# Optimization experiments

Hardware: AMD Instinct MI355X
Metric: run time of the kernel (lower is better)

## Reference

```python
import jax, jax.numpy as jnp
import numpy as np

MU_P = 0.15
MASK_ID = 103
VOCAB = 30522


def setup_inputs() -> dict:
    key = jax.random.key(0)
    k1, k2 = jax.random.split(key)
    B, C, S = 1024, 4, 2048
    # first half = per-token sampling weights, second half = shared_tokens (unused by the math)
    my_attention_mask = jax.random.uniform(k1, (B, C, 2 * S), dtype=jnp.float32)
    attention_mask = jnp.ones((B, C, S), dtype=jnp.int32)  # tokenizer attention mask
    input_ids = jax.random.randint(k2, (B, C, S), 0, VOCAB, dtype=jnp.int32)
    return {"my_attention_mask": my_attention_mask,
            "attention_mask": attention_mask,
            "input_ids": input_ids}


def reference(my_attention_mask, attention_mask, input_ids):
    """Weighted sampling WITHOUT replacement per (batch, choice) row via Gumbel-top-k.

    Original loops over (k, j), draws num_to_mask = floor(sum(tok_mask) * N(mu_p, sigma))
    indices from the nonzero weights in my_attention_mask[..., :S] (prob ~ weight),
    masks those token positions in input_ids and emits the indicator mask.
    Gumbel-top-k: keys = log(w) + Gumbel noise; the top-num_to_mask keys are a
    weighted sample without replacement from w. Zero-weight positions get -inf keys.
    """
    B, C, S = input_ids.shape
    w = my_attention_mask[..., :S]  # [B, C, S] sampling weights

    key = jax.random.key(42)
    kg, kn = jax.random.split(key)
    sigma = min(0.05, MU_P / 4.0)
    frac = MU_P + sigma * jax.random.normal(kn, (B, C), dtype=jnp.float32)
    num_to_mask = jnp.floor(
        attention_mask.sum(axis=-1).astype(jnp.float32) * frac
    ).astype(jnp.int32)  # [B, C]

    log_w = jnp.where(w > 0, jnp.log(jnp.maximum(w, 1e-30)), -jnp.inf)
    keys = log_w + jax.random.gumbel(kg, w.shape, dtype=jnp.float32)  # [B, C, S]

    # rank[i] = position of i in descending key order (double argsort)
    order = jnp.argsort(-keys, axis=-1)
    rank = jnp.argsort(order, axis=-1)
    new_attention_mask = (rank < num_to_mask[..., None]).astype(jnp.int32)  # [B, C, S]

    new_input_ids = jnp.where(new_attention_mask == 1, MASK_ID, input_ids)
    discriminator_labels = -new_attention_mask
    return new_input_ids, new_attention_mask, discriminator_labels
```

## Files before the change

kernel.cpp:

```cpp
#include <hip/hip_runtime.h>
#include <stdint.h>
#include <math.h>

#define SLEN 2048
#define EPT 16
#define NTHREADS 128
#define CPW 4
#define TOKENS_PER_OUT 8388608

__host__ __device__ __forceinline__ void tf2x32(uint32_t k0, uint32_t k1,
                                                uint32_t x0, uint32_t x1,
                                                uint32_t &o0, uint32_t &o1) {
  uint32_t ks2 = 0x1BD11BDAu ^ k0 ^ k1;
  x0 += k0; x1 += k1;
#define TFR(r) { x0 += x1; x1 = (x1 << (r)) | (x1 >> (32 - (r))); x1 ^= x0; }
  TFR(13) TFR(15) TFR(26) TFR(6)
  x0 += k1;  x1 += ks2 + 1u;
  TFR(17) TFR(29) TFR(16) TFR(24)
  x0 += ks2; x1 += k0 + 2u;
  TFR(13) TFR(15) TFR(26) TFR(6)
  x0 += k0;  x1 += k1 + 3u;
  TFR(17) TFR(29) TFR(16) TFR(24)
  x0 += k1;  x1 += ks2 + 4u;
  TFR(13) TFR(15) TFR(26) TFR(6)
  x0 += ks2; x1 += k0 + 5u;
#undef TFR
  o0 = x0; o1 = x1;
}

__device__ __forceinline__ void tf4_bits(uint32_t k0, uint32_t k1,
                                         uint32_t cbase, uint32_t bits[4]) {
  const uint32_t ks2 = 0x1BD11BDAu ^ k0 ^ k1;
  uint32_t x0[4], x1[4];
#pragma unroll
  for (int i = 0; i < 4; ++i) { x0[i] = k0; x1[i] = (cbase + (uint32_t)i) + k1; }
#define TFR4(r)                                                         \
  _Pragma("unroll")                                                     \
  for (int i = 0; i < 4; ++i) {                                         \
    x0[i] += x1[i];                                                     \
    x1[i] = (x1[i] << (r)) | (x1[i] >> (32 - (r)));                     \
    x1[i] ^= x0[i];                                                     \
  }                                                                     \
  __builtin_amdgcn_sched_barrier(0);
#define INJ4(a, b)                                                      \
  _Pragma("unroll")                                                     \
  for (int i = 0; i < 4; ++i) { x0[i] += (a); x1[i] += (b); }
  TFR4(13) TFR4(15) TFR4(26) TFR4(6)
  INJ4(k1, ks2 + 1u)
  TFR4(17) TFR4(29) TFR4(16) TFR4(24)
  INJ4(ks2, k0 + 2u)
  TFR4(13) TFR4(15) TFR4(26) TFR4(6)
  INJ4(k0, k1 + 3u)
  TFR4(17) TFR4(29) TFR4(16) TFR4(24)
  INJ4(k1, ks2 + 4u)
  TFR4(13) TFR4(15) TFR4(26) TFR4(6)
  INJ4(ks2, k0 + 5u)
#undef TFR4
#undef INJ4
#pragma unroll
  for (int i = 0; i < 4; ++i) bits[i] = x0[i] ^ x1[i];
}

__device__ __forceinline__ float u01_from_bits(uint32_t bits) {
  return __uint_as_float((bits >> 9) | 0x3F800000u) - 1.0f;
}

#define SBAR() __builtin_amdgcn_sched_barrier(0)

__device__ __forceinline__ void log8_cr(const float x[8], float out[8]) {
#pragma clang fp contract(off)
  double m[8]; int e[8];
#pragma unroll
  for (int i = 0; i < 8; ++i) {
    uint32_t xb   = __float_as_uint(x[i]);
    uint32_t mant = xb & 0x7FFFFFu;
    int      ee   = (int)(xb >> 23) - 127;
    bool     big  = mant > 0x3504F3u;
    e[i] = ee + (big ? 1 : 0);
    uint32_t hi = (big ? 0x3FE00000u : 0x3FF00000u) | (mant >> 3);
    uint32_t lo = mant << 29;
    m[i] = __longlong_as_double(((long long)hi << 32) | (long long)lo);
  }
  SBAR();
  double mp1[8];
#pragma unroll
  for (int i = 0; i < 8; ++i) mp1[i] = m[i] + 1.0;
  SBAR();
  double y[8];
#pragma unroll
  for (int i = 0; i < 8; ++i) y[i] = __builtin_amdgcn_rcp(mp1[i]);
  SBAR();
#pragma unroll
  for (int i = 0; i < 8; ++i) y[i] = fma(fma(-mp1[i], y[i], 1.0), y[i], y[i]);
  SBAR();
  double r[8];
#pragma unroll
  for (int i = 0; i < 8; ++i) r[i] = (m[i] - 1.0) * y[i];
  SBAR();
  double t[8];
#pragma unroll
  for (int i = 0; i < 8; ++i) t[i] = r[i] * r[i];
  SBAR();
  double p[8];
#pragma unroll
  for (int i = 0; i < 8; ++i) p[i] = fma(0.07692307692307693, t[i], 0.09090909090909091);
  SBAR();
#pragma unroll
  for (int i = 0; i < 8; ++i) p[i] = fma(p[i], t[i], 0.1111111111111111);
  SBAR();
#pragma unroll
  for (int i = 0; i < 8; ++i) p[i] = fma(p[i], t[i], 0.14285714285714285);
  SBAR();
#pragma unroll
  for (int i = 0; i < 8; ++i) p[i] = fma(p[i], t[i], 0.2);
  SBAR();
#pragma unroll
  for (int i = 0; i < 8; ++i) p[i] = fma(p[i], t[i], 0.3333333333333333);
  SBAR();
#pragma unroll
  for (int i = 0; i < 8; ++i) p[i] = fma(p[i], t[i], 1.0);
  SBAR();
#pragma unroll
  for (int i = 0; i < 8; ++i) r[i] = r[i] + r[i];
  SBAR();
#pragma unroll
  for (int i = 0; i < 8; ++i) p[i] = r[i] * p[i];
  SBAR();
#pragma unroll
  for (int i = 0; i < 8; ++i)
    out[i] = (float)fma((double)e[i], 0.6931471805599453, p[i]);
}

__device__ __forceinline__ float log_cr(float x) {
#pragma clang fp contract(off)
  uint32_t xb   = __float_as_uint(x);
  uint32_t mant = xb & 0x7FFFFFu;
  int      e    = (int)(xb >> 23) - 127;
  bool     big  = mant > 0x3504F3u;
  e += big ? 1 : 0;
  uint32_t hi = (big ? 0x3FE00000u : 0x3FF00000u) | (mant >> 3);
  double m = __longlong_as_double(((long long)hi << 32) | (long long)(mant << 29));
  double mp1 = m + 1.0;
  double y = __builtin_amdgcn_rcp(mp1);
  y = fma(fma(-mp1, y, 1.0), y, y);
  double r = (m - 1.0) * y;
  double t = r * r;
  double p = fma(0.07692307692307693, t, 0.09090909090909091);
  p = fma(p, t, 0.1111111111111111);
  p = fma(p, t, 0.14285714285714285);
  p = fma(p, t, 0.2);
  p = fma(p, t, 0.3333333333333333);
  p = fma(p, t, 1.0);
  return (float)fma((double)e, 0.6931471805599453, (r + r) * p);
}

__device__ float erfinv_xla(float x) {
#pragma clang fp contract(off)
  float x2  = x * x;
  float nx2 = -x2;
  float l1p;
  if (fabsf(nx2) < 1e-4f) {
    l1p = (-0.5f * nx2 + 1.0f) * nx2;
  } else {
    l1p = log_cr(1.0f + nx2);
  }
  float w = -l1p;
  float p;
  if (w < 5.0f) {
    float ww = w - 2.5f;
    p = 2.81022636e-08f;
    p = p * ww + 3.43273939e-07f;
    p = p * ww + -3.5233877e-06f;
    p = p * ww + -4.39150654e-06f;
    p = p * ww + 0.00021858087f;
    p = p * ww + -0.00125372503f;
    p = p * ww + -0.00417768164f;
    p = p * ww + 0.246640727f;
    p = p * ww + 1.50140941f;
  } else {
    float ww = sqrtf(w) - 3.0f;
    p = -0.000200214257f;
    p = p * ww + 0.000100950558f;
    p = p * ww + 0.00134934322f;
    p = p * ww + -0.00367342844f;
    p = p * ww + 0.00573950773f;
    p = p * ww + -0.0076224613f;
    p = p * ww + 0.00943887047f;
    p = p * ww + 1.00167406f;
    p = p * ww + 2.83297682f;
  }
  return p * x;
}

__global__ __launch_bounds__(NTHREADS, 8)
void gumbel_topk_mask(const float* __restrict__ wfull,
                      const int*   __restrict__ attn,
                      const int*   __restrict__ ids,
                      int* __restrict__ out,
                      uint32_t kg0, uint32_t kg1, uint32_t kn0, uint32_t kn1) {
#pragma clang fp contract(off)
  const int t    = threadIdx.x;
  const int lane = t & 63;
  const int wid  = t >> 6;
  const int row  = blockIdx.x;

  __shared__ __align__(16) uint32_t hist[2][256];
  __shared__ uint32_t wsum[2];
  __shared__ uint32_t wtot[2];

  const size_t rbase = (size_t)row * SLEN;
  const size_t wbase = (size_t)row * (2 * SLEN);

  ((uint2*)hist[0])[64 * wid + lane] = make_uint2(0u, 0u);

  const int4*   av4 = (const int4*)(attn + rbase);
  const float4* wv4 = (const float4*)(wfull + wbase);
  const int4*   iv4 = (const int4*)(ids + rbase);

  int psum = 0;
#pragma unroll
  for (int j = 0; j < CPW; ++j) {
    int4 a = av4[64 * (CPW * wid + j) + lane];
    psum += a.x + a.y + a.z + a.w;
  }

  uint32_t no0, no1;
  tf2x32(kn0, kn1, 0u, (uint32_t)row, no0, no1);
  float f0  = u01_from_bits(no0 ^ no1);
  float lo  = __uint_as_float(0xBF7FFFFFu);
  float u2  = fmaxf(lo, f0 * 2.0f + lo);
  float z   = erfinv_xla(u2);
  float nrm = 1.4142135623730951f * z;
  float frac = 0.15f + 0.0375f * nrm;

#pragma unroll
  for (int off = 32; off; off >>= 1) psum += __shfl_down(psum, off, 64);
  if (lane == 0) wsum[wid] = (uint32_t)psum;

  uint32_t mloc[EPT];
#pragma unroll
  for (int c = 0; c < 2; ++c) {
    const int g0 = CPW * wid + 2 * c;
    float4 wa = wv4[64 * g0 + lane];
    float4 wb = wv4[64 * (g0 + 1) + lane];
    uint32_t bits[8];
    tf4_bits(kg0, kg1, (uint32_t)(rbase + 256 * g0 + 4 * lane), bits + 0);
    tf4_bits(kg0, kg1, (uint32_t)(rbase + 256 * (g0 + 1) + 4 * lane), bits + 4);
    SBAR();
    float wl[8] = {wa.x, wa.y, wa.z, wa.w, wb.x, wb.y, wb.z, wb.w};
    float uu[8];
#pragma unroll
    for (int e = 0; e < 8; ++e) {
      float f = u01_from_bits(bits[e]);
      uu[e] = fmaxf(1.17549435e-38f, f * 1.0f + 1.17549435e-38f);
    }
    SBAR();
    float l1[8];
    log8_cr(uu, l1);
    float wm[8];
#pragma unroll
    for (int e = 0; e < 8; ++e) wm[e] = fmaxf(wl[e], 1e-30f);
    float lw[8];
    log8_cr(wm, lw);
    float nl1[8];
#pragma unroll
    for (int e = 0; e < 8; ++e) nl1[e] = -l1[e];
    float l2[8];
    log8_cr(nl1, l2);
    SBAR();
#pragma unroll
    for (int e = 0; e < 8; ++e) {
      float key = (wl[e] > 0.0f) ? (lw[e] + (-l2[e])) : -__builtin_inff();
      uint32_t kb = __float_as_uint(key);
      mloc[8 * c + e] = (kb & 0x80000000u) ? ~kb : (kb | 0x80000000u);
    }
  }

  int4 idsv[CPW];
#pragma unroll
  for (int j = 0; j < CPW; ++j) idsv[j] = iv4[64 * (CPW * wid + j) + lane];

  __syncthreads();
  int asum = (int)(wsum[0] + wsum[1]);
  int kk = (int)floorf((float)asum * frac);

  uint32_t T, r;
  if (kk <= 0)          { T = 0xFFFFFFFFu; r = 0u; }
  else if (kk >= SLEN)  { T = 0u;          r = (uint32_t)SLEN; }
  else {
    T = 0u;
    uint32_t need = (uint32_t)kk;
#pragma unroll
    for (int e = 0; e < EPT; ++e)
      atomicAdd(&hist[0][mloc[e] >> 24], 1u);
    int cur = 0;
    for (int p = 3; ; --p) {
      __syncthreads();
      uint4 hq = ((const uint4*)hist[cur])[lane];
      ((uint2*)hist[cur ^ 1])[64 * wid + lane] = make_uint2(0u, 0u);
      uint32_t gs  = hq.x + hq.y + hq.z + hq.w;
      uint32_t sfx = gs;
#pragma unroll
      for (int off = 1; off < 64; off <<= 1) {
        uint32_t n = __shfl_down(sfx, off, 64);
        if (lane + off < 64) sfx += n;
      }
      uint32_t Gex = sfx - gs;
      uint32_t S3 = Gex;
      uint32_t S2 = S3 + hq.w;
      uint32_t S1 = S2 + hq.z;
      uint32_t S0 = S1 + hq.y;
      uint32_t hh[4] = {hq.x, hq.y, hq.z, hq.w};
      uint32_t SS[4] = {S0, S1, S2, S3};
      int haswin = 0; uint32_t binv = 0u, remv = 0u; int donev = 0;
#pragma unroll
      for (int i = 0; i < 4; ++i) {
        if (hh[i] && SS[i] < need && need <= SS[i] + hh[i]) {
          haswin = 1;
          binv = (uint32_t)(4 * lane + i);
          remv = need - SS[i];
          donev = (remv == hh[i]) ? 1 : 0;
        }
      }
      unsigned long long wmask = __ballot(haswin);
      int src = (int)(__ffsll((unsigned long long)wmask) - 1);
      uint32_t bin = (uint32_t)__shfl((int)binv, src, 64);
      uint32_t rem = (uint32_t)__shfl((int)remv, src, 64);
      int     done = __shfl(donev, src, 64);
      T |= bin << (8 * p);
      need = rem;
      if (done || p == 0) { r = rem; break; }
      __syncthreads();
      const int sh = 8 * p;
#pragma unroll
      for (int e = 0; e < EPT; ++e) {
        uint32_t m = mloc[e];
        if ((m >> sh) == (T >> sh))
          atomicAdd(&hist[cur ^ 1][(m >> (sh - 8)) & 255u], 1u);
      }
      cur ^= 1;
    }
  }

  uint32_t cnt[CPW];
#pragma unroll
  for (int j = 0; j < CPW; ++j) {
    uint32_t c = 0;
#pragma unroll
    for (int e = 0; e < 4; ++e) c += (mloc[4 * j + e] == T) ? 1u : 0u;
    cnt[j] = c;
  }
  uint32_t incl[2];
#pragma unroll
  for (int q = 0; q < 2; ++q) incl[q] = cnt[2 * q] | (cnt[2 * q + 1] << 16);
#pragma unroll
  for (int off = 1; off < 64; off <<= 1) {
#pragma unroll
    for (int q = 0; q < 2; ++q) {
      uint32_t n = __shfl_up(incl[q], off, 64);
      if (lane >= off) incl[q] += n;
    }
  }
  uint32_t Spre[CPW], tot[CPW];
#pragma unroll
  for (int q = 0; q < 2; ++q) {
    uint32_t t63 = (uint32_t)__shfl((int)incl[q], 63, 64);
    tot[2 * q]      = t63 & 0xFFFFu;
    tot[2 * q + 1]  = t63 >> 16;
    Spre[2 * q]     = (incl[q] & 0xFFFFu) - cnt[2 * q];
    Spre[2 * q + 1] = (incl[q] >> 16)     - cnt[2 * q + 1];
  }
  if (lane == 0) wtot[wid] = tot[0] + tot[1] + tot[2] + tot[3];
  __syncthreads();
  uint32_t C = wid ? wtot[0] : 0u;

  int4* po = (int4*)(out + rbase);
  int4* pm = (int4*)(out + TOKENS_PER_OUT + rbase);
  int4* pl = (int4*)(out + 2 * TOKENS_PER_OUT + rbase);
#pragma unroll
  for (int j = 0; j < CPW; ++j) {
    uint32_t excl = C + Spre[j];
    int4 iv = idsv[j];
    int idv[4] = {iv.x, iv.y, iv.z, iv.w};
    int oid[4], omk[4], olb[4];
#pragma unroll
    for (int e = 0; e < 4; ++e) {
      uint32_t m = mloc[4 * j + e];
      bool eq  = (m == T);
      bool msk = (m > T) || (eq && (excl < r));
      excl += eq ? 1u : 0u;
      oid[e] = msk ? 103 : idv[e];
      omk[e] = msk ? 1 : 0;
      olb[e] = msk ? -1 : 0;
    }
    const int gi = 64 * (CPW * wid + j) + lane;
    po[gi] = make_int4(oid[0], oid[1], oid[2], oid[3]);
    pm[gi] = make_int4(omk[0], omk[1], omk[2], omk[3]);
    pl[gi] = make_int4(olb[0], olb[1], olb[2], olb[3]);
    C += tot[j];
  }
}

extern "C" void kernel_launch(void* const* d_in, const int* in_sizes, int n_in,
                              void* d_out, int out_size, void* d_ws, size_t ws_size,
                              hipStream_t stream) {
  (void)n_in; (void)d_ws; (void)ws_size; (void)out_size;
  const float* wfull = (const float*)d_in[0];
  const int*   attn  = (const int*)d_in[1];
  const int*   ids   = (const int*)d_in[2];
  int* out = (int*)d_out;

  uint32_t kg0, kg1, kn0, kn1, o0, o1;
  tf2x32(0u, 42u, 0u, 0u, o0, o1); kg0 = o0; kg1 = o1;
  tf2x32(0u, 42u, 0u, 1u, o0, o1); kn0 = o0; kn1 = o1;

  int rows = in_sizes[1] / SLEN;
  hipLaunchKernelGGL(gumbel_topk_mask, dim3(rows), dim3(NTHREADS),
                     0, stream, wfull, attn, ids, out, kg0, kg1, kn0, kn1);
}
```

Before: 213.1 us.

## Process four rows per wave pair with register prefetch of next row

Each block now runs two independent wave pairs, each handling four consecutive rows. The inputs for the next row are prefetched into registers while the current row is being computed. The intent is to hide global load latency and to amortise launch and block setup. The cost is more register pressure, with launch bounds dropped to 2 blocks, and fewer blocks overall (1024 rows / 8 = 512), which risks lower occupancy and block-wide barriers shared across both pairs.

```diff
diff --git a/kernel.cpp b/kernel.cpp
--- a/kernel.cpp
+++ b/kernel.cpp
@@ -4,8 +4,9 @@
 
 #define SLEN 2048
 #define EPT 16
-#define NTHREADS 128
+#define NTHREADS 256
 #define CPW 4
+#define DSEQ 4
 #define TOKENS_PER_OUT 8388608
 
 __host__ __device__ __forceinline__ void tf2x32(uint32_t k0, uint32_t k1,
@@ -192,7 +193,7 @@
   return p * x;
 }
 
-__global__ __launch_bounds__(NTHREADS, 8)
+__global__ __launch_bounds__(NTHREADS, 2)
 void gumbel_topk_mask(const float* __restrict__ wfull,
                       const int*   __restrict__ attn,
                       const int*   __restrict__ ids,
@@ -202,202 +203,237 @@
   const int t    = threadIdx.x;
   const int lane = t & 63;
   const int wid  = t >> 6;
-  const int row  = blockIdx.x;
-
-  __shared__ __align__(16) uint32_t hist[2][256];
-  __shared__ uint32_t wsum[2];
-  __shared__ uint32_t wtot[2];
-
-  const size_t rbase = (size_t)row * SLEN;
-  const size_t wbase = (size_t)row * (2 * SLEN);
-
-  ((uint2*)hist[0])[64 * wid + lane] = make_uint2(0u, 0u);
-
-  const int4*   av4 = (const int4*)(attn + rbase);
-  const float4* wv4 = (const float4*)(wfull + wbase);
-  const int4*   iv4 = (const int4*)(ids + rbase);
-
-  int psum = 0;
-#pragma unroll
-  for (int j = 0; j < CPW; ++j) {
-    int4 a = av4[64 * (CPW * wid + j) + lane];
-    psum += a.x + a.y + a.z + a.w;
+  const int pid  = wid >> 1;
+  const int wl   = wid & 1;
+
+  __shared__ __align__(16) uint32_t hist[2][2][256];
+  __shared__ uint32_t wsum[2][2];
+  __shared__ uint32_t wtot[2][2];
+
+  const int row0 = (blockIdx.x * 2 + pid) * DSEQ;
+
+  int4 attnC[CPW]; float4 wC[CPW]; int4 idsC[CPW];
+  {
+    const size_t rb = (size_t)row0 * SLEN;
+    const int4*   av4 = (const int4*)(attn + rb);
+    const float4* wv4 = (const float4*)(wfull + 2 * rb);
+    const int4*   iv4 = (const int4*)(ids + rb);
+#pragma unroll
+    for (int j = 0; j < CPW; ++j) {
+      attnC[j] = av4[64 * (CPW * wl + j) + lane];
+      wC[j]    = wv4[64 * (CPW * wl + j) + lane];
+      idsC[j]  = iv4[64 * (CPW * wl + j) + lane];
+    }
   }
 
-  uint32_t no0, no1;
-  tf2x32(kn0, kn1, 0u, (uint32_t)row, no0, no1);
-  float f0  = u01_from_bits(no0 ^ no1);
-  float lo  = __uint_as_float(0xBF7FFFFFu);
-  float u2  = fmaxf(lo, f0 * 2.0f + lo);
-  float z   = erfinv_xla(u2);
-  float nrm = 1.4142135623730951f * z;
-  float frac = 0.15f + 0.0375f * nrm;
-
-#pragma unroll
-  for (int off = 32; off; off >>= 1) psum += __shfl_down(psum, off, 64);
-  if (lane == 0) wsum[wid] = (uint32_t)psum;
-
-  uint32_t mloc[EPT];
-#pragma unroll
-  for (int c = 0; c < 2; ++c) {
-    const int g0 = CPW * wid + 2 * c;
-    float4 wa = wv4[64 * g0 + lane];
-    float4 wb = wv4[64 * (g0 + 1) + lane];
-    uint32_t bits[8];
-    tf4_bits(kg0, kg1, (uint32_t)(rbase + 256 * g0 + 4 * lane), bits + 0);
-    tf4_bits(kg0, kg1, (uint32_t)(rbase + 256 * (g0 + 1) + 4 * lane), bits + 4);
-    SBAR();
-    float wl[8] = {wa.x, wa.y, wa.z, wa.w, wb.x, wb.y, wb.z, wb.w};
-    float uu[8];
-#pragma unroll
-    for (int e = 0; e < 8; ++e) {
-      float f = u01_from_bits(bits[e]);
-      uu[e] = fmaxf(1.17549435e-38f, f * 1.0f + 1.17549435e-38f);
-    }
-    SBAR();
-    float l1[8];
-    log8_cr(uu, l1);
-    float wm[8];
-#pragma unroll
-    for (int e = 0; e < 8; ++e) wm[e] = fmaxf(wl[e], 1e-30f);
-    float lw[8];
-    log8_cr(wm, lw);
-    float nl1[8];
-#pragma unroll
-    for (int e = 0; e < 8; ++e) nl1[e] = -l1[e];
-    float l2[8];
-    log8_cr(nl1, l2);
-    SBAR();
-#pragma unroll
-    for (int e = 0; e < 8; ++e) {
-      float key = (wl[e] > 0.0f) ? (lw[e] + (-l2[e])) : -__builtin_inff();
-      uint32_t kb = __float_as_uint(key);
-      mloc[8 * c + e] = (kb & 0x80000000u) ? ~kb : (kb | 0x80000000u);
-    }
-  }
-
-  int4 idsv[CPW];
-#pragma unroll
-  for (int j = 0; j < CPW; ++j) idsv[j] = iv4[64 * (CPW * wid + j) + lane];
-
-  __syncthreads();
-  int asum = (int)(wsum[0] + wsum[1]);
-  int kk = (int)floorf((float)asum * frac);
-
-  uint32_t T, r;
-  if (kk <= 0)          { T = 0xFFFFFFFFu; r = 0u; }
-  else if (kk >= SLEN)  { T = 0u;          r = (uint32_t)SLEN; }
-  else {
-    T = 0u;
-    uint32_t need = (uint32_t)kk;
-#pragma unroll
-    for (int e = 0; e < EPT; ++e)
-      atomicAdd(&hist[0][mloc[e] >> 24], 1u);
+  for (int rr = 0; rr < DSEQ; ++rr) {
+    const int row = row0 + rr;
+    const size_t rbase = (size_t)row * SLEN;
+
+    int4 attnN[CPW]; float4 wN[CPW]; int4 idsN[CPW];
+    if (rr < DSEQ - 1) {
+      const size_t rbN = rbase + SLEN;
+      const int4*   av4 = (const int4*)(attn + rbN);
+      const float4* wv4 = (const float4*)(wfull + 2 * rbN);
+      const int4*   iv4 = (const int4*)(ids + rbN);
+#pragma unroll
+      for (int j = 0; j < CPW; ++j) {
+        attnN[j] = av4[64 * (CPW * wl + j) + lane];
+        wN[j]    = wv4[64 * (CPW * wl + j) + lane];
+        idsN[j]  = iv4[64 * (CPW * wl + j) + lane];
+      }
+    }
+
+    ((uint2*)hist[pid][0])[64 * wl + lane] = make_uint2(0u, 0u);
+
+    int psum = 0;
+#pragma unroll
+    for (int j = 0; j < CPW; ++j)
+      psum += attnC[j].x + attnC[j].y + attnC[j].z + attnC[j].w;
+
+    uint32_t no0, no1;
+    tf2x32(kn0, kn1, 0u, (uint32_t)row, no0, no1);
+    float f0  = u01_from_bits(no0 ^ no1);
+    float lo  = __uint_as_float(0xBF7FFFFFu);
+    float u2  = fmaxf(lo, f0 * 2.0f + lo);
+    float z   = erfinv_xla(u2);
+    float nrm = 1.4142135623730951f * z;
+    float frac = 0.15f + 0.0375f * nrm;
+
+#pragma unroll
+    for (int off = 32; off; off >>= 1) psum += __shfl_down(psum, off, 64);
+    if (lane == 0) wsum[pid][wl] = (uint32_t)psum;
+
+    uint32_t mloc[EPT];
+#pragma unroll
+    for (int c = 0; c < 2; ++c) {
+      const int g0 = CPW * wl + 2 * c;
+      float4 wa = wC[2 * c], wb = wC[2 * c + 1];
+      uint32_t bits[8];
+      tf4_bits(kg0, kg1, (uint32_t)(rbase + 256 * g0 + 4 * lane), bits + 0);
+      tf4_bits(kg0, kg1, (uint32_t)(rbase + 256 * (g0 + 1) + 4 * lane), bits + 4);
+      SBAR();
+      float wl8[8] = {wa.x, wa.y, wa.z, wa.w, wb.x, wb.y, wb.z, wb.w};
+      float uu[8];
+#pragma unroll
+      for (int e = 0; e < 8; ++e) {
+        float f = u01_from_bits(bits[e]);
+        uu[e] = fmaxf(1.17549435e-38f, f * 1.0f + 1.17549435e-38f);
+      }
+      SBAR();
+      float l1[8];
+      log8_cr(uu, l1);
+      float wm[8];
+#pragma unroll
+      for (int e = 0; e < 8; ++e) wm[e] = fmaxf(wl8[e], 1e-30f);
+      float lw[8];
+      log8_cr(wm, lw);
+      float nl1[8];
+#pragma unroll
+      for (int e = 0; e < 8; ++e) nl1[e] = -l1[e];
+      float l2[8];
+      log8_cr(nl1, l2);
+      SBAR();
+#pragma unroll
+      for (int e = 0; e < 8; ++e) {
+        float key = (wl8[e] > 0.0f) ? (lw[e] + (-l2[e])) : -__builtin_inff();
+        uint32_t kb = __float_as_uint(key);
+        mloc[8 * c + e] = (kb & 0x80000000u) ? ~kb : (kb | 0x80000000u);
+      }
+    }
+
+    __syncthreads();
+    int asum = (int)(wsum[pid][0] + wsum[pid][1]);
+    int kk = (int)floorf((float)asum * frac);
+
+    uint32_t T = 0u, r = 0u, need = 0u;
+    bool doneF = false;
+    if (kk <= 0)          { T = 0xFFFFFFFFu; r = 0u; doneF = true; }
+    else if (kk >= SLEN)  { T = 0u; r = (uint32_t)SLEN; doneF = true; }
+    else {
+      need = (uint32_t)kk;
+#pragma unroll
+      for (int e = 0; e < EPT; ++e)
+        atomicAdd(&hist[pid][0][mloc[e] >> 24], 1u);
+    }
     int cur = 0;
-    for (int p = 3; ; --p) {
+    for (int p = 3; p >= 0; --p) {
       __syncthreads();
-      uint4 hq = ((const uint4*)hist[cur])[lane];
-      ((uint2*)hist[cur ^ 1])[64 * wid + lane] = make_uint2(0u, 0u);
-      uint32_t gs  = hq.x + hq.y + hq.z + hq.w;
-      uint32_t sfx = gs;
-#pragma unroll
-      for (int off = 1; off < 64; off <<= 1) {
-        uint32_t n = __shfl_down(sfx, off, 64);
-        if (lane + off < 64) sfx += n;
-      }
-      uint32_t Gex = sfx - gs;
-      uint32_t S3 = Gex;
-      uint32_t S2 = S3 + hq.w;
-      uint32_t S1 = S2 + hq.z;
-      uint32_t S0 = S1 + hq.y;
-      uint32_t hh[4] = {hq.x, hq.y, hq.z, hq.w};
-      uint32_t SS[4] = {S0, S1, S2, S3};
-      int haswin = 0; uint32_t binv = 0u, remv = 0u; int donev = 0;
-#pragma unroll
-      for (int i = 0; i < 4; ++i) {
-        if (hh[i] && SS[i] < need && need <= SS[i] + hh[i]) {
-          haswin = 1;
-          binv = (uint32_t)(4 * lane + i);
-          remv = need - SS[i];
-          donev = (remv == hh[i]) ? 1 : 0;
+      if (!doneF) {
+        uint4 hq = ((const uint4*)hist[pid][cur])[lane];
+        ((uint2*)hist[pid][cur ^ 1])[64 * wl + lane] = make_uint2(0u, 0u);
+        uint32_t gs  = hq.x + hq.y + hq.z + hq.w;
+        uint32_t sfx = gs;
+#pragma unroll
+        for (int off = 1; off < 64; off <<= 1) {
+          uint32_t n = __shfl_down(sfx, off, 64);
+          if (lane + off < 64) sfx += n;
         }
-      }
-      unsigned long long wmask = __ballot(haswin);
-      int src = (int)(__ffsll((unsigned long long)wmask) - 1);
-      uint32_t bin = (uint32_t)__shfl((int)binv, src, 64);
-      uint32_t rem = (uint32_t)__shfl((int)remv, src, 64);
-      int     done = __shfl(donev, src, 64);
-      T |= bin << (8 * p);
-      need = rem;
-      if (done || p == 0) { r = rem; break; }
+        uint32_t Gex = sfx - gs;
+        uint32_t S3 = Gex;
+        uint32_t S2 = S3 + hq.w;
+        uint32_t S1 = S2 + hq.z;
+        uint32_t S0 = S1 + hq.y;
+        uint32_t hh[4] = {hq.x, hq.y, hq.z, hq.w};
+        uint32_t SS[4] = {S0, S1, S2, S3};
+        int haswin = 0; uint32_t binv = 0u, remv = 0u; int donev = 0;
+#pragma unroll
+        for (int i = 0; i < 4; ++i) {
+          if (hh[i] && SS[i] < need && need <= SS[i] + hh[i]) {
+            haswin = 1;
+            binv = (uint32_t)(4 * lane + i);
+            remv = need - SS[i];
+            donev = (remv == hh[i]) ? 1 : 0;
+          }
+        }
+        unsigned long long wmask = __ballot(haswin);
+        int src = (int)(__ffsll((unsigned long long)wmask) - 1);
+        uint32_t bin = (uint32_t)__shfl((int)binv, src, 64);
+        uint32_t rem = (uint32_t)__shfl((int)remv, src, 64);
+        int     done = __shfl(donev, src, 64);
+        T |= bin << (8 * p);
+        need = rem;
+        if (done || p == 0) { r = rem; doneF = true; }
+      }
       __syncthreads();
-      const int sh = 8 * p;
-#pragma unroll
-      for (int e = 0; e < EPT; ++e) {
-        uint32_t m = mloc[e];
-        if ((m >> sh) == (T >> sh))
-          atomicAdd(&hist[cur ^ 1][(m >> (sh - 8)) & 255u], 1u);
+      if (!doneF && p > 0) {
+        const int sh = 8 * p;
+#pragma unroll
+        for (int e = 0; e < EPT; ++e) {
+          uint32_t m = mloc[e];
+          if ((m >> sh) == (T >> sh))
+            atomicAdd(&hist[pid][cur ^ 1][(m >> (sh - 8)) & 255u], 1u);
+        }
       }
       cur ^= 1;
     }
-  }
-
-  uint32_t cnt[CPW];
-#pragma unroll
-  for (int j = 0; j < CPW; ++j) {
-    uint32_t c = 0;
-#pragma unroll
-    for (int e = 0; e < 4; ++e) c += (mloc[4 * j + e] == T) ? 1u : 0u;
-    cnt[j] = c;
-  }
-  uint32_t incl[2];
-#pragma unroll
-  for (int q = 0; q < 2; ++q) incl[q] = cnt[2 * q] | (cnt[2 * q + 1] << 16);
-#pragma unroll
-  for (int off = 1; off < 64; off <<= 1) {
+
+    uint32_t cnt[CPW];
+#pragma unroll
+    for (int j = 0; j < CPW; ++j) {
+      uint32_t c = 0;
+#pragma unroll
+      for (int e = 0; e < 4; ++e) c += (mloc[4 * j + e] == T) ? 1u : 0u;
+      cnt[j] = c;
+    }
+    uint32_t incl[2];
+#pragma unroll
+    for (int q = 0; q < 2; ++q) incl[q] = cnt[2 * q] | (cnt[2 * q + 1] << 16);
+#pragma unroll
+    for (int off = 1; off < 64; off <<= 1) {
+#pragma unroll
+      for (int q = 0; q < 2; ++q) {
+        uint32_t n = __shfl_up(incl[q], off, 64);
+        if (lane >= off) incl[q] += n;
+      }
+    }
+    uint32_t Spre[CPW], tot[CPW];
 #pragma unroll
     for (int q = 0; q < 2; ++q) {
-      uint32_t n = __shfl_up(incl[q], off, 64);
-      if (lane >= off) incl[q] += n;
-    }
-  }
-  uint32_t Spre[CPW], tot[CPW];
-#pragma unroll
-  for (int q = 0; q < 2; ++q) {
-    uint32_t t63 = (uint32_t)__shfl((int)incl[q], 63, 64);
-    tot[2 * q]      = t63 & 0xFFFFu;
-    tot[2 * q + 1]  = t63 >> 16;
-    Spre[2 * q]     = (incl[q] & 0xFFFFu) - cnt[2 * q];
-    Spre[2 * q + 1] = (incl[q] >> 16)     - cnt[2 * q + 1];
-  }
-  if (lane == 0) wtot[wid] = tot[0] + tot[1] + tot[2] + tot[3];
-  __syncthreads();
-  uint32_t C = wid ? wtot[0] : 0u;
-
-  int4* po = (int4*)(out + rbase);
-  int4* pm = (int4*)(out + TOKENS_PER_OUT + rbase);
-  int4* pl = (int4*)(out + 2 * TOKENS_PER_OUT + rbase);
-#pragma unroll
-  for (int j = 0; j < CPW; ++j) {
-    uint32_t excl = C + Spre[j];
-    int4 iv = idsv[j];
-    int idv[4] = {iv.x, iv.y, iv.z, iv.w};
-    int oid[4], omk[4], olb[4];
-#pragma unroll
-    for (int e = 0; e < 4; ++e) {
-      uint32_t m = mloc[4 * j + e];
-      bool eq  = (m == T);
-      bool msk = (m > T) || (eq && (excl < r));
-      excl += eq ? 1u : 0u;
-      oid[e] = msk ? 103 : idv[e];
-      omk[e] = msk ? 1 : 0;
-      olb[e] = msk ? -1 : 0;
-    }
-    const int gi = 64 * (CPW * wid + j) + lane;
-    po[gi] = make_int4(oid[0], oid[1], oid[2], oid[3]);
-    pm[gi] = make_int4(omk[0], omk[1], omk[2], omk[3]);
-    pl[gi] = make_int4(olb[0], olb[1], olb[2], olb[3]);
-    C += tot[j];
+      uint32_t t63 = (uint32_t)__shfl((int)incl[q], 63, 64);
+      tot[2 * q]      = t63 & 0xFFFFu;
+      tot[2 * q + 1]  = t63 >> 16;
+      Spre[2 * q]     = (incl[q] & 0xFFFFu) - cnt[2 * q];
+      Spre[2 * q + 1] = (incl[q] >> 16)     - cnt[2 * q + 1];
+    }
+    if (lane == 0) wtot[pid][wl] = tot[0] + tot[1] + tot[2] + tot[3];
+    __syncthreads();
+    uint32_t C = wl ? wtot[pid][0] : 0u;
+
+    int4* po = (int4*)(out + rbase);
+    int4* pm = (int4*)(out + TOKENS_PER_OUT + rbase);
+    int4* pl = (int4*)(out + 2 * TOKENS_PER_OUT + rbase);
+#pragma unroll
+    for (int j = 0; j < CPW; ++j) {
+      uint32_t excl = C + Spre[j];
+      int4 iv = idsC[j];
+      int idv[4] = {iv.x, iv.y, iv.z, iv.w};
+      int oid[4], omk[4], olb[4];
+#pragma unroll
+      for (int e = 0; e < 4; ++e) {
+        uint32_t m = mloc[4 * j + e];
+        bool eq  = (m == T);
+        bool msk = (m > T) || (eq && (excl < r));
+        excl += eq ? 1u : 0u;
+        oid[e] = msk ? 103 : idv[e];
+        omk[e] = msk ? 1 : 0;
+        olb[e] = msk ? -1 : 0;
+      }
+      const int gi = 64 * (CPW * wl + j) + lane;
+      po[gi] = make_int4(oid[0], oid[1], oid[2], oid[3]);
+      pm[gi] = make_int4(omk[0], omk[1], omk[2], omk[3]);
+      pl[gi] = make_int4(olb[0], olb[1], olb[2], olb[3]);
+      C += tot[j];
+    }
+
+    if (rr < DSEQ - 1) {
+#pragma unroll
+      for (int j = 0; j < CPW; ++j) {
+        attnC[j] = attnN[j];
+        wC[j]    = wN[j];
+        idsC[j]  = idsN[j];
+      }
+    }
   }
 }
 
@@ -415,6 +451,6 @@
   tf2x32(0u, 42u, 0u, 1u, o0, o1); kn0 = o0; kn1 = o1;
 
   int rows = in_sizes[1] / SLEN;
-  hipLaunchKernelGGL(gumbel_topk_mask, dim3(rows), dim3(NTHREADS),
+  hipLaunchKernelGGL(gumbel_topk_mask, dim3(rows / (2 * DSEQ)), dim3(NTHREADS),
                      0, stream, wfull, attn, ids, out, kg0, kg1, kn0, kn1);
 }
```

Result: slower. 237.0 us (+11.2%).
